# Kernel optimization log

Measured on AMD Instinct MI355X. Metric: run time of the kernel, lower is better.

## Reference

```python
import jax, jax.numpy as jnp
import numpy as np

MIN_RATIO, MAX_RATIO = 0.7, 1.3
MIN_BIAS, MAX_BIAS = -4.0, 4.0
SOFTMAX_SCALE = 3.0


def setup_inputs() -> dict:
    key = jax.random.key(0)
    k1, k2, k3 = jax.random.split(key, 3)
    B, L_org, N = 32, 2048, 21
    org_tensor = jax.random.normal(k1, (B, L_org, N), dtype=jnp.float32)
    # small perturbations so the clamps are active but not saturated
    ratio_minus_one = 0.1 * jax.random.normal(k2, (N,), dtype=jnp.float32)
    bias = 0.5 * jax.random.normal(k3, (N,), dtype=jnp.float32)
    return {"org_tensor": org_tensor, "ratio_minus_one": ratio_minus_one,
            "bias": bias, "to_length": 2048}


def reference(org_tensor, ratio_minus_one, bias, to_length):
    # input_transformation with is_mark=False
    B, L_org, N = org_tensor.shape
    L_to = to_length
    dt = org_tensor.dtype
    # relu-based clamping in the original == clip
    ratio = jnp.clip(ratio_minus_one + 1.0, MIN_RATIO, MAX_RATIO)  # [N]
    b = jnp.clip(bias, MIN_BIAS, MAX_BIAS)                         # [N]
    org_pos = jnp.arange(-L_org, 0, dtype=dt)                      # [L_org]
    # transformed positions are batch-independent: [L_org, N, 1]
    tpos = org_pos[:, None, None] * ratio[None, :, None] + b[None, :, None]
    tgt = jnp.arange(-L_to, 0, dtype=dt)                           # [L_to]
    deltas = (tpos - tgt[None, None, :]) ** 2                      # [L_org, N, L_to]
    weights = jax.nn.softmax(-deltas * SOFTMAX_SCALE, axis=0)      # softmax over L_org
    # einsum 'bont,bon->btn' with batch-independent weights
    out = jnp.einsum('ont,bon->btn', weights, org_tensor)          # [B, L_to, N]
    return out
```

## Files before the change

### kernel.cpp

```cpp
#include <hip/hip_runtime.h>
#include <hip/hip_bf16.h>


constexpr int LORG  = 2048;
constexpr int LTO   = 2048;
constexpr int NCH   = 21;
constexpr int BATCH = 32;
constexpr int W     = 8;
constexpr int NW    = 2 * W + 1;
constexpr int TT    = 64;
constexpr int BH    = 8;
constexpr int NBLK  = NCH * (LTO / TT) * (BATCH / BH);

constexpr float MIN_RATIO = 0.7f, MAX_RATIO = 1.3f;
constexpr float MIN_BIAS  = -4.0f, MAX_BIAS = 4.0f;
constexpr float NEG3LOG2E = -3.0f * 1.4426950408889634f;

__device__ __forceinline__ int compute_o0(float tg, float bb, float ir) {
    const float ocf = (float)LORG + (tg - bb) * ir;
    int o0 = (int)floorf(ocf + 0.5f) - W;
    return max(0, min(LORG - NW, o0));
}

__global__ __launch_bounds__(256) void li_fused(
    const float* __restrict__ x,
    const float* __restrict__ rmo,
    const float* __restrict__ bias,
    float* __restrict__ out)
{
    const int h  = blockIdx.x;
    const int wk = (h & 7) * (NBLK / 8) + (h >> 3);
    const int bh = wk & 3;
    const int tn = wk >> 2;
    const int tt = tn / NCH;
    const int n  = tn - tt * NCH;
    const int t0 = tt * TT;

    const int tid = threadIdx.x;
    const int tl  = tid & 63;
    const int wv  = tid >> 6;
    const int b0  = bh * BH;

    __shared__ float xs[4][2][128];

    const float r  = fminf(fmaxf(rmo[n] + 1.0f, MIN_RATIO), MAX_RATIO);
    const float bb = fminf(fmaxf(bias[n], MIN_BIAS), MAX_BIAS);
    const float ir = 1.0f / r;

    const int lo  = compute_o0((float)(t0 - LTO), bb, ir);
    const int hi  = compute_o0((float)(t0 + TT - 1 - LTO), bb, ir);
    const int len = hi + NW - lo;

    const int i0 = min(tl,      len - 1);
    const int i1 = min(tl + 64, len - 1);

    const int bA = b0 + wv;
    const float* colA = x + ((size_t)((bA    ) * LORG + lo)) * NCH + n;
    const float* colB = x + ((size_t)((bA + 4) * LORG + lo)) * NCH + n;
    const float a0 = colA[(size_t)i0 * NCH], a1 = colA[(size_t)i1 * NCH];
    const float c0 = colB[(size_t)i0 * NCH], c1 = colB[(size_t)i1 * NCH];

    const float tg = (float)(t0 + tl - LTO);
    const int   o0 = compute_o0(tg, bb, ir);
    const int base = o0 - lo;
    float d = (float)(o0 - LORG) * r + bb - tg;
    float js = floorf(-d * ir + 0.5f);
    js = fminf(fmaxf(js, 0.0f), 16.0f);
    const float dstar = d + js * r;
    const float m = NEG3LOG2E * dstar * dstar;
    float w[NW];
    float s = 0.0f;
    #pragma unroll
    for (int j = 0; j < NW; ++j) {
        const float e = NEG3LOG2E * d * d - m;
        w[j] = exp2f(e);
        s += w[j];
        d += r;
    }
    const float inv = 1.0f / s;

    xs[wv][0][tl]      = a0;
    xs[wv][0][tl + 64] = a1;
    xs[wv][1][tl]      = c0;
    xs[wv][1][tl + 64] = c1;

    float accA = 0.0f, accB = 0.0f;
    #pragma unroll
    for (int j = 0; j < NW; ++j) {
        accA = fmaf(w[j], xs[wv][0][base + j], accA);
        accB = fmaf(w[j], xs[wv][1][base + j], accB);
    }
    out[((size_t)(bA    ) * LTO + t0 + tl) * NCH + n] = accA * inv;
    out[((size_t)(bA + 4) * LTO + t0 + tl) * NCH + n] = accB * inv;
}

extern "C" void kernel_launch(void* const* d_in, const int* in_sizes, int n_in,
                              void* d_out, int out_size, void* d_ws, size_t ws_size,
                              hipStream_t stream) {
    const float* x    = (const float*)d_in[0];
    const float* rmo  = (const float*)d_in[1];
    const float* bias = (const float*)d_in[2];
    float* out = (float*)d_out;

    li_fused<<<NBLK, 256, 0, stream>>>(x, rmo, bias, out);
}
```

Before: 16.32 us.

## Transpose input to channel-major workspace and interpolate all channels per block

Adds a pre-pass that transposes x from [B,L,N] into channel-major [N,B,L] in the workspace. A new interpolation kernel then loads contiguous windows per channel and computes all 21 channels for 32 target positions of one batch. It stages the outputs in shared memory so the [B,L,N] output is written with coalesced stores. This removes the strided 84-byte-stride gathers and scattered stores of the fused kernel. The cost is a second launch and an extra full round trip of the input through global memory, with the old kernel kept as a fallback when the workspace is too small.

```diff
diff --git a/kernel.cpp b/kernel.cpp
--- a/kernel.cpp
+++ b/kernel.cpp
@@ -8,9 +8,7 @@
 constexpr int BATCH = 32;
 constexpr int W     = 8;
 constexpr int NW    = 2 * W + 1;
-constexpr int TT    = 64;
-constexpr int BH    = 8;
-constexpr int NBLK  = NCH * (LTO / TT) * (BATCH / BH);
+constexpr int TT    = 32;
 
 constexpr float MIN_RATIO = 0.7f, MAX_RATIO = 1.3f;
 constexpr float MIN_BIAS  = -4.0f, MAX_BIAS = 4.0f;
@@ -22,35 +20,120 @@
     return max(0, min(LORG - NW, o0));
 }
 
+__global__ __launch_bounds__(256) void li_transpose(
+    const float* __restrict__ x, float* __restrict__ xt)
+{
+    const int b  = blockIdx.y;
+    const int o0 = blockIdx.x * 64;
+    __shared__ float tile[64 * NCH];
+    const float* src = x + ((size_t)b * LORG + o0) * NCH;
+    for (int i = threadIdx.x; i < 64 * NCH; i += 256) tile[i] = src[i];
+    __syncthreads();
+    for (int j = threadIdx.x; j < 64 * NCH; j += 256) {
+        const int n = j >> 6, k = j & 63;
+        xt[((size_t)(n * BATCH + b)) * LORG + o0 + k] = tile[k * NCH + n];
+    }
+}
+
+__global__ __launch_bounds__(256) void li_interp(
+    const float* __restrict__ xt,
+    const float* __restrict__ rmo,
+    const float* __restrict__ bias,
+    float* __restrict__ out)
+{
+    const int h  = blockIdx.x;
+    const int wk = (h & 7) * 256 + (h >> 3);
+    const int b  = wk >> 6;
+    const int tt = wk & 63;
+    const int t0 = tt * TT;
+
+    const int tid = threadIdx.x;
+
+    __shared__ float xs[NCH][64];
+    __shared__ float osh[TT * NCH];
+    __shared__ float rshv[NCH], bshv[NCH], irshv[NCH];
+    __shared__ int   lov[NCH], lenv[NCH];
+
+    if (tid < NCH) {
+        const float r  = fminf(fmaxf(rmo[tid] + 1.0f, MIN_RATIO), MAX_RATIO);
+        const float bb = fminf(fmaxf(bias[tid], MIN_BIAS), MAX_BIAS);
+        const float ir = 1.0f / r;
+        const int lo = compute_o0((float)(t0 - LTO), bb, ir);
+        const int hi = compute_o0((float)(t0 + TT - 1 - LTO), bb, ir);
+        rshv[tid]  = r;  bshv[tid] = bb;  irshv[tid] = ir;
+        lov[tid]   = lo;
+        lenv[tid]  = hi + NW - lo;
+    }
+    __syncthreads();
+
+    for (int idx = tid; idx < NCH * 64; idx += 256) {
+        const int n = idx >> 6, i = idx & 63;
+        const int ic = min(i, lenv[n] - 1);
+        xs[n][i] = xt[((size_t)n * BATCH + b) * LORG + lov[n] + ic];
+    }
+    __syncthreads();
+
+    const int tl = tid & 31;
+    const int cg = tid >> 5;
+    const float tg = (float)(t0 + tl - LTO);
+    #pragma unroll
+    for (int c = 0; c < 3; ++c) {
+        const int n = cg + 8 * c;
+        if (n < NCH) {
+            const float r  = rshv[n];
+            const float bb = bshv[n];
+            const float ir = irshv[n];
+            const int   o0 = compute_o0(tg, bb, ir);
+            const int base = o0 - lov[n];
+            float d = (float)(o0 - LORG) * r + bb - tg;
+            float js = floorf(-d * ir + 0.5f);
+            js = fminf(fmaxf(js, 0.0f), 16.0f);
+            const float dstar = d + js * r;
+            const float m = NEG3LOG2E * dstar * dstar;
+            float s = 0.0f, acc = 0.0f;
+            #pragma unroll
+            for (int j = 0; j < NW; ++j) {
+                const float wgt = exp2f(NEG3LOG2E * d * d - m);
+                s += wgt;
+                acc = fmaf(wgt, xs[n][base + j], acc);
+                d += r;
+            }
+            osh[tl * NCH + n] = acc * (1.0f / s);
+        }
+    }
+    __syncthreads();
+
+    float* dst = out + ((size_t)b * LTO + t0) * NCH;
+    for (int i = tid; i < TT * NCH; i += 256) dst[i] = osh[i];
+}
+
 __global__ __launch_bounds__(256) void li_fused(
     const float* __restrict__ x,
     const float* __restrict__ rmo,
     const float* __restrict__ bias,
     float* __restrict__ out)
 {
+    const int NB = NCH * (LTO / 64) * (BATCH / 8);
     const int h  = blockIdx.x;
-    const int wk = (h & 7) * (NBLK / 8) + (h >> 3);
+    const int wk = (h & 7) * (NB / 8) + (h >> 3);
     const int bh = wk & 3;
     const int tn = wk >> 2;
     const int tt = tn / NCH;
     const int n  = tn - tt * NCH;
-    const int t0 = tt * TT;
-
+    const int t0 = tt * 64;
     const int tid = threadIdx.x;
     const int tl  = tid & 63;
     const int wv  = tid >> 6;
-    const int b0  = bh * BH;
+    const int b0  = bh * 8;
 
     __shared__ float xs[4][2][128];
 
     const float r  = fminf(fmaxf(rmo[n] + 1.0f, MIN_RATIO), MAX_RATIO);
     const float bb = fminf(fmaxf(bias[n], MIN_BIAS), MAX_BIAS);
     const float ir = 1.0f / r;
-
     const int lo  = compute_o0((float)(t0 - LTO), bb, ir);
-    const int hi  = compute_o0((float)(t0 + TT - 1 - LTO), bb, ir);
+    const int hi  = compute_o0((float)(t0 + 63 - LTO), bb, ir);
     const int len = hi + NW - lo;
-
     const int i0 = min(tl,      len - 1);
     const int i1 = min(tl + 64, len - 1);
 
@@ -72,17 +155,14 @@
     float s = 0.0f;
     #pragma unroll
     for (int j = 0; j < NW; ++j) {
-        const float e = NEG3LOG2E * d * d - m;
-        w[j] = exp2f(e);
+        w[j] = exp2f(NEG3LOG2E * d * d - m);
         s += w[j];
         d += r;
     }
     const float inv = 1.0f / s;
 
-    xs[wv][0][tl]      = a0;
-    xs[wv][0][tl + 64] = a1;
-    xs[wv][1][tl]      = c0;
-    xs[wv][1][tl + 64] = c1;
+    xs[wv][0][tl] = a0; xs[wv][0][tl + 64] = a1;
+    xs[wv][1][tl] = c0; xs[wv][1][tl + 64] = c1;
 
     float accA = 0.0f, accB = 0.0f;
     #pragma unroll
@@ -102,5 +182,12 @@
     const float* bias = (const float*)d_in[2];
     float* out = (float*)d_out;
 
-    li_fused<<<NBLK, 256, 0, stream>>>(x, rmo, bias, out);
+    const size_t xt_bytes = (size_t)NCH * BATCH * LORG * sizeof(float);
+    if (ws_size >= xt_bytes) {
+        float* xt = (float*)d_ws;
+        li_transpose<<<dim3(LORG / 64, BATCH), 256, 0, stream>>>(x, xt);
+        li_interp<<<2048, 256, 0, stream>>>(xt, rmo, bias, out);
+    } else {
+        li_fused<<<2688, 256, 0, stream>>>(x, rmo, bias, out);
+    }
 }
```

Result: slower. 21.91 us (+34.2%).
